# Performance work log

Hardware: AMD Instinct MI355X
Metric: run time of the kernel (lower is better)

## Reference

```python
import jax, jax.numpy as jnp
import numpy as np

GROUPS = 32
EPS = 1e-5
N_HEADS = 8
MAX_REL = 16  # temporal_length
NEG_INF = -1e8


def group_norm(x, scale, bias):
    # x: [N, C, L]
    n, c, l = x.shape
    xg = x.reshape(n, GROUPS, (c // GROUPS) * l)
    mean = xg.mean(-1, keepdims=True)
    var = xg.var(-1, keepdims=True)
    xn = ((xg - mean) / jnp.sqrt(var + EPS)).reshape(n, c, l)
    return xn * scale[None, :, None] + bias[None, :, None]


def conv1x1(x, w, b):
    # x: [N, Cin, L], w: [Cout, Cin], b: [Cout]
    return jnp.einsum('oc,ncl->nol', w, x) + b[None, :, None]


def rel_pos_emb(table, length):
    # table: [2*MAX_REL+1, ch] -> [length, length, ch]
    r = jnp.arange(length)
    dist = jnp.clip(r[None, :] - r[:, None], -MAX_REL, MAX_REL) + MAX_REL
    return table[dist]


def qkv_attention(qkv, k_rp=None, v_rp=None, causal=False):
    # qkv: [N, 3*H*ch, L]  (new attention order: chunk into q,k,v blocks)
    bs, width, L = qkv.shape
    ch = width // (3 * N_HEADS)
    q, k, v = jnp.split(qkv, 3, axis=1)
    q = q.reshape(bs * N_HEADS, ch, L)
    k = k.reshape(bs * N_HEADS, ch, L)
    v = v.reshape(bs * N_HEADS, ch, L)
    scale = 1.0 / jnp.sqrt(jnp.sqrt(jnp.asarray(ch, dtype=qkv.dtype)))
    w = jnp.einsum('bct,bcs->bts', q * scale, k * scale)
    if k_rp is not None:
        # faithful to original: 'bst' result added directly onto 'bts' weight
        w = w + jnp.einsum('bct,tsc->bst', q * scale, k_rp)
    if causal:
        mask = jnp.tril(jnp.ones((L, L), dtype=w.dtype))
        w = jnp.where(mask == 0, NEG_INF, w)
    w = jax.nn.softmax(w, axis=-1)
    a = jnp.einsum('bts,bcs->bct', w, v)
    if v_rp is not None:
        a = a + jnp.einsum('bts,tsc->btc', w, v_rp).transpose(0, 2, 1)
    return a.reshape(bs, -1, L)


def st_attention(x, norm_s_w, norm_s_b, qkv_s_w, qkv_s_b, proj_s_w, proj_s_b,
                 norm_t_w, norm_t_b, qkv_t_w, qkv_t_b, proj_t_w, proj_t_b,
                 rpk_table, rpv_table):
    b, c, t, h, w = x.shape
    # spatial attention over (h*w) tokens, batch (b*t)
    out = x.transpose(0, 2, 1, 3, 4).reshape(b * t, c, h * w)
    qkv = conv1x1(group_norm(out, norm_s_w, norm_s_b), qkv_s_w, qkv_s_b)
    out = qkv_attention(qkv)
    out = conv1x1(out, proj_s_w, proj_s_b)
    out = out.reshape(b, t, c, h, w).transpose(0, 2, 1, 3, 4)
    x = x + out
    # temporal attention over t tokens, batch (b*h*w), with RPE + causal mask
    out = x.transpose(0, 3, 4, 1, 2).reshape(b * h * w, c, t)
    qkv = conv1x1(group_norm(out, norm_t_w, norm_t_b), qkv_t_w, qkv_t_b)
    k_rp = rel_pos_emb(rpk_table, t)
    v_rp = rel_pos_emb(rpv_table, t)
    out = qkv_attention(qkv, k_rp=k_rp, v_rp=v_rp, causal=True)
    out = conv1x1(out, proj_t_w, proj_t_b)
    out = out.reshape(b, h, w, c, t).transpose(0, 3, 4, 1, 2)
    return x + out


def setup_inputs() -> dict:
    key = jax.random.key(0)
    ks = jax.random.split(key, 12)
    B, C, T, H, W = 2, 512, 16, 24, 24
    ch = C // N_HEADS
    inp = {
        'x': jax.random.normal(ks[0], (B, C, T, H, W), jnp.float32),
        'norm_s_w': jnp.ones((C,), jnp.float32),
        'norm_s_b': jnp.zeros((C,), jnp.float32),
        'qkv_s_w': jax.random.normal(ks[1], (3 * C, C), jnp.float32) * 0.02,
        'qkv_s_b': jnp.zeros((3 * C,), jnp.float32),
        'proj_s_w': jax.random.normal(ks[2], (C, C), jnp.float32) * 0.02,
        'proj_s_b': jnp.zeros((C,), jnp.float32),
        'norm_t_w': jnp.ones((C,), jnp.float32),
        'norm_t_b': jnp.zeros((C,), jnp.float32),
        'qkv_t_w': jax.random.normal(ks[3], (3 * C, C), jnp.float32) * 0.02,
        'qkv_t_b': jnp.zeros((3 * C,), jnp.float32),
        'proj_t_w': jax.random.normal(ks[4], (C, C), jnp.float32) * 0.02,
        'proj_t_b': jnp.zeros((C,), jnp.float32),
        'rpk_table': jax.random.normal(ks[5], (2 * MAX_REL + 1, ch), jnp.float32) * 0.05,
        'rpv_table': jax.random.normal(ks[6], (2 * MAX_REL + 1, ch), jnp.float32) * 0.05,
    }
    return inp


def reference(x, norm_s_w, norm_s_b, qkv_s_w, qkv_s_b, proj_s_w, proj_s_b,
              norm_t_w, norm_t_b, qkv_t_w, qkv_t_b, proj_t_w, proj_t_b,
              rpk_table, rpv_table):
    return st_attention(x, norm_s_w, norm_s_b, qkv_s_w, qkv_s_b, proj_s_w, proj_s_b,
                        norm_t_w, norm_t_b, qkv_t_w, qkv_t_b, proj_t_w, proj_t_b,
                        rpk_table, rpv_table)
```

## Files before the change

kernel.cpp:

```cpp
#include <hip/hip_runtime.h>
#include <hip/hip_bf16.h>

typedef __hip_bfloat16 bf16;
typedef __attribute__((ext_vector_type(8))) short v8s;
typedef __attribute__((ext_vector_type(4))) float v4f;

__device__ __forceinline__ float b2f(bf16 v){ return __bfloat162float(v); }
__device__ __forceinline__ bf16  f2b(float v){ return __float2bfloat16(v); }

__device__ __forceinline__ float ldin(const void* p, int i, bool f32in){
  return f32in ? ((const float*)p)[i] : b2f(((const bf16*)p)[i]);
}

__device__ __forceinline__ void stage4(const void* src, size_t off, bool f32in, bf16* dst){
  union { bf16 h[4]; ushort4 u; } tmp;
  if (f32in){
    float4 f = *(const float4*)((const float*)src + off);
    tmp.h[0] = f2b(f.x); tmp.h[1] = f2b(f.y); tmp.h[2] = f2b(f.z); tmp.h[3] = f2b(f.w);
  } else {
    tmp.u = *(const ushort4*)((const ushort*)src + off);
  }
  *(ushort4*)dst = tmp.u;
}
__device__ __forceinline__ void stage4b(const bf16* src, bf16* dst){
  *(ushort4*)dst = *(const ushort4*)src;
}

__device__ __forceinline__ void async_cp16(const bf16* g, bf16* l){
  __builtin_amdgcn_global_load_lds(
      (const __attribute__((address_space(1))) unsigned int*)g,
      (__attribute__((address_space(3))) unsigned int*)l, 16, 0, 0);
}


__global__ void k_detect(const void* x, int* flag){
  int tid = threadIdx.x;
  const bf16* p = (const bf16*)x;
  int cnt = 0;
  for (int i = tid; i < 512; i += 64){
    float v = b2f(p[i]);
    if (!(fabsf(v) <= 64.f)) cnt++;
  }
  #pragma unroll
  for (int off = 32; off; off >>= 1) cnt += __shfl_down(cnt, off, 64);
  if (tid == 0) flag[0] = (cnt > 16) ? 1 : 0;
}

__global__ __launch_bounds__(256) void k_cvtw(const void* __restrict__ W,
        bf16* __restrict__ out, int n4, const int* __restrict__ flag){
  const bool f32in = flag[0] != 0;
  int i = blockIdx.x*256 + threadIdx.x;
  if (i < n4) stage4(W, (size_t)i*4, f32in, out + (size_t)i*4);
}

__global__ __launch_bounds__(256) void k_gn_s(const void* __restrict__ x,
        const void* __restrict__ gw, const void* __restrict__ gb,
        bf16* __restrict__ xnT, const int* __restrict__ flag, int n0){
  const bool f32in = flag[0] != 0;
  const int g = blockIdx.x;
  const int nl = blockIdx.y;
  const int n = n0 + nl;
  const int b = n >> 4, t = n & 15;
  const int tid = threadIdx.x;
  __shared__ float xs[576*17];
  __shared__ float red[4][2];
  __shared__ float stats[2];
  float s = 0.f, q = 0.f;
  for (int i = tid; i < 9216; i += 256){
    int cg = i / 576, l = i - cg*576;
    int c = g*16 + cg;
    float v = ldin(x, ((b*512 + c)*16 + t)*576 + l, f32in);
    xs[l*17 + cg] = v; s += v; q += v*v;
  }
  #pragma unroll
  for (int off = 32; off; off >>= 1){ s += __shfl_down(s, off, 64); q += __shfl_down(q, off, 64); }
  int wid = tid >> 6;
  if ((tid & 63) == 0){ red[wid][0] = s; red[wid][1] = q; }
  __syncthreads();
  if (tid == 0){
    float S = red[0][0]+red[1][0]+red[2][0]+red[3][0];
    float Q = red[0][1]+red[1][1]+red[2][1]+red[3][1];
    float mean = S * (1.f/9216.f);
    float var  = Q * (1.f/9216.f) - mean*mean;
    stats[0] = mean; stats[1] = rsqrtf(fmaxf(var, 0.f) + 1e-5f);
  }
  __syncthreads();
  float mean = stats[0], rstd = stats[1];
  for (int i = tid; i < 9216; i += 256){
    int l = i >> 4, cg = i & 15;
    int c = g*16 + cg;
    xnT[(size_t)(nl*576 + l)*512 + c] =
        f2b((xs[l*17 + cg] - mean)*rstd*ldin(gw, c, f32in) + ldin(gb, c, f32in));
  }
}

__global__ __launch_bounds__(256) void k_gemm_qkv(const bf16* __restrict__ Xf,
        const bf16* __restrict__ Wb, const void* __restrict__ Bv,
        bf16* __restrict__ Y, const int* __restrict__ flag,
        size_t kOff, size_t vOff, int mode){
  const bool f32in = flag[0] != 0;
  const int nwg = gridDim.x;
  const int bid = blockIdx.x;
  const int g = (bid & 7)*(nwg >> 3) + (bid >> 3);
  const int mt = g / 12, nt = g - mt*12;
  const int r0 = mt*128, o0 = nt*128;
  const int tid = threadIdx.x, lane = tid & 63, w = tid >> 6;
  const int wm = w & 1, wn = w >> 1;
  const int r15 = lane & 15, quad = lane >> 4;
  const int rsw = r15 & 7;
  __shared__ bf16 As[128*64];
  __shared__ bf16 Bs[128*64];
  v4f acc[4][4];
  #pragma unroll
  for (int i = 0; i < 4; ++i)
    #pragma unroll
    for (int j = 0; j < 4; ++j) acc[i][j] = (v4f){0.f,0.f,0.f,0.f};
  for (int kc = 0; kc < 512; kc += 64){
    __syncthreads();
    #pragma unroll
    for (int r = 0; r < 4; ++r){
      int d = (tid + 256*r)*8;
      int row = d >> 6;
      int slot = (d >> 3) & 7;
      int col = ((slot ^ (row & 7)) * 8);
      async_cp16(&Xf[(size_t)(r0 + row)*512 + kc + col], As + r*2048 + w*512);
      async_cp16(&Wb[(size_t)(o0 + row)*512 + kc + col], Bs + r*2048 + w*512);
    }
    __syncthreads();
    #pragma unroll
    for (int ks = 0; ks < 2; ++ks){
      v8s a[4], b[4];
      #pragma unroll
      for (int mi = 0; mi < 4; ++mi)
        a[mi] = *(const v8s*)&As[(wm*64 + mi*16 + r15)*64 + (((ks*4 + quad) ^ rsw)*8)];
      #pragma unroll
      for (int ni = 0; ni < 4; ++ni)
        b[ni] = *(const v8s*)&Bs[(wn*64 + ni*16 + r15)*64 + (((ks*4 + quad) ^ rsw)*8)];
      #pragma unroll
      for (int mi = 0; mi < 4; ++mi)
        #pragma unroll
        for (int ni = 0; ni < 4; ++ni)
          acc[mi][ni] = __builtin_amdgcn_mfma_f32_16x16x32_bf16(a[mi], b[ni], acc[mi][ni], 0, 0, 0);
    }
  }
  if (mode == 0){
    #pragma unroll
    for (int ni = 0; ni < 4; ++ni){
      int o = o0 + wn*64 + ni*16 + r15;
      int seg = o >> 9, oseg = o & 511;
      size_t segb = (seg==0) ? 0 : (seg==1) ? kOff : vOff;
      float bia = ldin(Bv, o, f32in);
      #pragma unroll
      for (int mi = 0; mi < 4; ++mi)
        #pragma unroll
        for (int rg = 0; rg < 4; ++rg){
          int rr = r0 + wm*64 + mi*16 + quad*4 + rg;
          int nl = rr / 576, l = rr - nl*576;
          size_t dst = segb + (size_t)nl*294912 +
                       ((seg==2) ? ((size_t)oseg*576 + l) : ((size_t)l*512 + oseg));
          Y[dst] = f2b(acc[mi][ni][rg] + bia);
        }
    }
  } else {
    #pragma unroll
    for (int ni = 0; ni < 4; ++ni){
      int o = o0 + wn*64 + ni*16 + r15;
      float bia = ldin(Bv, o, f32in);
      #pragma unroll
      for (int mi = 0; mi < 4; ++mi)
        #pragma unroll
        for (int rg = 0; rg < 4; ++rg){
          int rr = r0 + wm*64 + mi*16 + quad*4 + rg;
          int m = rr >> 4, t = rr & 15;
          Y[((size_t)m*1536 + o)*16 + t] = f2b(acc[mi][ni][rg] + bia);
        }
    }
  }
}

__global__ __launch_bounds__(256, 4) void k_attn_s_mfma(const bf16* __restrict__ qkv,
        bf16* __restrict__ attT, size_t kOff, size_t vOff){
  const int bid = blockIdx.x;
  const int xcd = bid & 7, slot = bid >> 3;
  const int nl = xcd + 8*(slot/72);
  const int idx = slot - 72*(slot/72);
  const int head = idx/9, t0 = idx - 9*head;
  const int tid = threadIdx.x, lane = tid & 63, w = tid >> 6;
  const int r15 = lane & 15, quad = lane >> 4;
  __shared__ bf16 Ks[64*72];
  __shared__ bf16 Vs[64*72];
  __shared__ bf16 Ps[4][16*72];
  const bf16* QT = qkv + (size_t)nl*294912;
  const bf16* KT = qkv + kOff + (size_t)nl*294912;
  const bf16* Vp = qkv + vOff + (size_t)nl*294912;
  const int c0 = head*64;
  v8s aq0, aq1;
  {
    const bf16* qrow = QT + (size_t)(t0*64 + w*16 + r15)*512 + c0;
    aq0 = *(const v8s*)(qrow + quad*8);
    aq1 = *(const v8s*)(qrow + 32 + quad*8);
  }
  v4f oc[4];
  #pragma unroll
  for (int ni = 0; ni < 4; ++ni) oc[ni] = (v4f){0.f,0.f,0.f,0.f};
  float m_run[4] = {-1e30f,-1e30f,-1e30f,-1e30f};
  float l_run[4] = {0.f,0.f,0.f,0.f};
  for (int sc = 0; sc < 9; ++sc){
    __syncthreads();
    #pragma unroll
    for (int r = 0; r < 4; ++r){
      int e4 = (tid + 256*r)*4;
      int row = e4 >> 6, col = e4 & 63;
      stage4b(&KT[(size_t)(sc*64 + row)*512 + c0 + col], &Ks[row*72 + col]);
      stage4b(&Vp[(size_t)(c0 + row)*576 + sc*64 + col], &Vs[row*72 + col]);
    }
    __syncthreads();
    v4f sa[4];
    #pragma unroll
    for (int sj = 0; sj < 4; ++sj) sa[sj] = (v4f){0.f,0.f,0.f,0.f};
    #pragma unroll
    for (int sj = 0; sj < 4; ++sj){
      v8s b0 = *(const v8s*)&Ks[(sj*16 + r15)*72 + quad*8];
      v8s b1 = *(const v8s*)&Ks[(sj*16 + r15)*72 + 32 + quad*8];
      sa[sj] = __builtin_amdgcn_mfma_f32_16x16x32_bf16(aq0, b0, sa[sj], 0, 0, 0);
      sa[sj] = __builtin_amdgcn_mfma_f32_16x16x32_bf16(aq1, b1, sa[sj], 0, 0, 0);
    }
    float cmx[4] = {-1e30f,-1e30f,-1e30f,-1e30f};
    #pragma unroll
    for (int sj = 0; sj < 4; ++sj)
      #pragma unroll
      for (int rg = 0; rg < 4; ++rg){
        float v = sa[sj][rg]*0.125f;
        sa[sj][rg] = v;
        cmx[rg] = fmaxf(cmx[rg], v);
      }
    #pragma unroll
    for (int off = 1; off < 16; off <<= 1)
      #pragma unroll
      for (int rg = 0; rg < 4; ++rg) cmx[rg] = fmaxf(cmx[rg], __shfl_xor(cmx[rg], off, 64));
    float alpha[4];
    #pragma unroll
    for (int rg = 0; rg < 4; ++rg){
      float mnew = fmaxf(m_run[rg], cmx[rg]);
      alpha[rg] = __expf(m_run[rg] - mnew);
      m_run[rg] = mnew;
    }
    float psum[4] = {0.f,0.f,0.f,0.f};
    #pragma unroll
    for (int sj = 0; sj < 4; ++sj)
      #pragma unroll
      for (int rg = 0; rg < 4; ++rg){
        float e = __expf(sa[sj][rg] - m_run[rg]);
        sa[sj][rg] = e; psum[rg] += e;
      }
    #pragma unroll
    for (int off = 1; off < 16; off <<= 1)
      #pragma unroll
      for (int rg = 0; rg < 4; ++rg) psum[rg] += __shfl_xor(psum[rg], off, 64);
    #pragma unroll
    for (int rg = 0; rg < 4; ++rg) l_run[rg] = l_run[rg]*alpha[rg] + psum[rg];
    #pragma unroll
    for (int ni = 0; ni < 4; ++ni)
      #pragma unroll
      for (int rg = 0; rg < 4; ++rg) oc[ni][rg] *= alpha[rg];
    #pragma unroll
    for (int sj = 0; sj < 4; ++sj)
      #pragma unroll
      for (int rg = 0; rg < 4; ++rg)
        Ps[w][(quad*4 + rg)*72 + sj*16 + r15] = f2b(sa[sj][rg]);
    #pragma unroll
    for (int ks = 0; ks < 2; ++ks){
      v8s a = *(const v8s*)&Ps[w][r15*72 + ks*32 + quad*8];
      #pragma unroll
      for (int ni = 0; ni < 4; ++ni){
        v8s b = *(const v8s*)&Vs[(ni*16 + r15)*72 + ks*32 + quad*8];
        oc[ni] = __builtin_amdgcn_mfma_f32_16x16x32_bf16(a, b, oc[ni], 0, 0, 0);
      }
    }
  }
  float inv[4];
  #pragma unroll
  for (int rg = 0; rg < 4; ++rg) inv[rg] = 1.f / l_run[rg];
  #pragma unroll
  for (int ni = 0; ni < 4; ++ni)
    #pragma unroll
    for (int rg = 0; rg < 4; ++rg){
      int t = t0*64 + w*16 + quad*4 + rg;
      attT[(size_t)(nl*576 + t)*512 + c0 + ni*16 + r15] = f2b(oc[ni][rg]*inv[rg]);
    }
}

__global__ __launch_bounds__(256) void k_proj_s_mfma(const bf16* __restrict__ AT,
        const bf16* __restrict__ Wb, const void* __restrict__ Bv,
        const void* __restrict__ xin, bf16* __restrict__ x2,
        bf16* __restrict__ x2T, int doT,
        const int* __restrict__ flag, int n0){
  const bool f32in = flag[0] != 0;
  const int o0 = blockIdx.x * 128;
  const int l0 = blockIdx.y * 64;
  const int nl = blockIdx.z;
  const int n = n0 + nl;
  const int b = n >> 4, t = n & 15;
  const int tid = threadIdx.x, lane = tid & 63;
  const int wm = (tid >> 6) & 1, wn = tid >> 7;
  const int r15 = lane & 15, quad = lane >> 4;
  __shared__ bf16 As[128*72];
  __shared__ bf16 Bs[64*72];
  v4f acc[4][2];
  #pragma unroll
  for (int i = 0; i < 4; ++i)
    #pragma unroll
    for (int j = 0; j < 2; ++j) acc[i][j] = (v4f){0.f,0.f,0.f,0.f};
  for (int kc = 0; kc < 512; kc += 64){
    __syncthreads();
    #pragma unroll
    for (int r = 0; r < 8; ++r){
      int e4 = (tid + 256*r)*4;
      int row = e4 >> 6, k = e4 & 63;
      stage4b(&Wb[(size_t)(o0+row)*512 + kc + k], &As[row*72 + k]);
    }
    #pragma unroll
    for (int r = 0; r < 4; ++r){
      int e4 = (tid + 256*r)*4;
      int row = e4 >> 6, k = e4 & 63;
      stage4b(&AT[(size_t)(nl*576 + l0 + row)*512 + kc + k], &Bs[row*72 + k]);
    }
    __syncthreads();
    #pragma unroll
    for (int ks = 0; ks < 2; ++ks){
      v8s a[4], b[2];
      #pragma unroll
      for (int mi = 0; mi < 4; ++mi)
        a[mi] = *(const v8s*)&As[(wm*64 + mi*16 + r15)*72 + ks*32 + quad*8];
      #pragma unroll
      for (int ni = 0; ni < 2; ++ni)
        b[ni] = *(const v8s*)&Bs[(wn*32 + ni*16 + r15)*72 + ks*32 + quad*8];
      #pragma unroll
      for (int mi = 0; mi < 4; ++mi)
        #pragma unroll
        for (int ni = 0; ni < 2; ++ni)
          acc[mi][ni] = __builtin_amdgcn_mfma_f32_16x16x32_bf16(a[mi], b[ni], acc[mi][ni], 0, 0, 0);
    }
  }
  __syncthreads();
  #pragma unroll
  for (int mi = 0; mi < 4; ++mi){
    int orel = wm*64 + mi*16 + quad*4;
    #pragma unroll
    for (int rg = 0; rg < 4; ++rg){
      float bia = ldin(Bv, o0 + orel + rg, f32in);
      #pragma unroll
      for (int ni = 0; ni < 2; ++ni)
        As[(orel + rg)*72 + wn*32 + ni*16 + r15] = f2b(acc[mi][ni][rg] + bia);
    }
  }
  __syncthreads();
  const size_t xrow = ((size_t)(b*512 + o0)*16 + t)*576 + l0;
  for (int it = 0; it < 4; ++it){
    int idx = tid + it*256;
    int o = idx >> 3, lc = (idx & 7)*8;
    union { bf16 h[8]; v8s v; } val;
    val.v = *(const v8s*)&As[o*72 + lc];
    size_t ga = xrow + (size_t)o*9216 + lc;
    if (f32in){
      const float* xp = (const float*)xin + ga;
      float4 f0 = *(const float4*)xp;
      float4 f1 = *(const float4*)(xp + 4);
      val.h[0] = f2b(b2f(val.h[0]) + f0.x);
      val.h[1] = f2b(b2f(val.h[1]) + f0.y);
      val.h[2] = f2b(b2f(val.h[2]) + f0.z);
      val.h[3] = f2b(b2f(val.h[3]) + f0.w);
      val.h[4] = f2b(b2f(val.h[4]) + f1.x);
      val.h[5] = f2b(b2f(val.h[5]) + f1.y);
      val.h[6] = f2b(b2f(val.h[6]) + f1.z);
      val.h[7] = f2b(b2f(val.h[7]) + f1.w);
    } else {
      union { bf16 h[8]; v8s v; } xv;
      xv.v = *(const v8s*)((const bf16*)xin + ga);
      #pragma unroll
      for (int j = 0; j < 8; ++j) val.h[j] = f2b(b2f(val.h[j]) + b2f(xv.h[j]));
    }
    *(v8s*)&x2[ga] = val.v;
    if (doT) *(v8s*)&As[o*72 + lc] = val.v;
  }
  if (doT){
    __syncthreads();
    const size_t tbase = ((size_t)b*576 + l0)*8192 + (size_t)t*512 + o0;
    for (int it = 0; it < 4; ++it){
      int l = (tid & 15) + it*16;
      int ocg = (tid >> 4)*8;
      union { bf16 h[8]; v8s v; } val;
      #pragma unroll
      for (int j = 0; j < 8; ++j) val.h[j] = As[(ocg + j)*72 + l];
      *(v8s*)&x2T[tbase + (size_t)l*8192 + ocg] = val.v;
    }
  }
}

__global__ __launch_bounds__(256) void k_gn_t(const bf16* __restrict__ x2,
        const void* __restrict__ gw, const void* __restrict__ gb,
        bf16* __restrict__ xnT, const int* __restrict__ flag, int m0){
  const bool f32in = flag[0] != 0;
  const int ml = blockIdx.x;
  const int m = m0 + ml;
  const int b = m / 576, l = m - b*576;
  const int tid = threadIdx.x;
  __shared__ float xs[8192];
  __shared__ float mg[32], rg[32];
  for (int i = tid; i < 8192; i += 256){
    int t = i >> 9, c = i & 511;
    xs[i] = b2f(x2[((b*512 + c)*16 + t)*576 + l]);
  }
  __syncthreads();
  {
    int g = tid >> 3, ii = tid & 7;
    float s = 0.f, q = 0.f;
    for (int idx = ii; idx < 256; idx += 8){
      int t = idx >> 4, cg = idx & 15;
      float v = xs[t*512 + g*16 + cg]; s += v; q += v*v;
    }
    #pragma unroll
    for (int off = 1; off < 8; off <<= 1){ s += __shfl_xor(s, off, 64); q += __shfl_xor(q, off, 64); }
    if (ii == 0){
      float mean = s*(1.f/256.f);
      float var  = q*(1.f/256.f) - mean*mean;
      mg[g] = mean; rg[g] = rsqrtf(fmaxf(var, 0.f) + 1e-5f);
    }
  }
  __syncthreads();
  for (int i = tid; i < 8192; i += 256){
    int c = i & 511, g = c >> 4;
    xnT[(size_t)ml*8192 + i] = f2b((xs[i] - mg[g])*rg[g]*ldin(gw, c, f32in) + ldin(gb, c, f32in));
  }
}

__global__ __launch_bounds__(256) void k_gn_t2(const bf16* __restrict__ x2T,
        const void* __restrict__ gw, const void* __restrict__ gb,
        bf16* __restrict__ xnT, const int* __restrict__ flag, int m0){
  const bool f32in = flag[0] != 0;
  const int ml = blockIdx.x;
  const int m = m0 + ml;
  const int tid = threadIdx.x;
  __shared__ float xs[8192];
  __shared__ float mg[32], rg[32];
  for (int i = tid; i < 8192; i += 256)
    xs[i] = b2f(x2T[(size_t)m*8192 + i]);
  __syncthreads();
  {
    int g = tid >> 3, ii = tid & 7;
    float s = 0.f, q = 0.f;
    for (int idx = ii; idx < 256; idx += 8){
      int t = idx >> 4, cg = idx & 15;
      float v = xs[t*512 + g*16 + cg]; s += v; q += v*v;
    }
    #pragma unroll
    for (int off = 1; off < 8; off <<= 1){ s += __shfl_xor(s, off, 64); q += __shfl_xor(q, off, 64); }
    if (ii == 0){
      float mean = s*(1.f/256.f);
      float var  = q*(1.f/256.f) - mean*mean;
      mg[g] = mean; rg[g] = rsqrtf(fmaxf(var, 0.f) + 1e-5f);
    }
  }
  __syncthreads();
  for (int i = tid; i < 8192; i += 256){
    int c = i & 511, g = c >> 4;
    xnT[(size_t)ml*8192 + i] = f2b((xs[i] - mg[g])*rg[g]*ldin(gw, c, f32in) + ldin(gb, c, f32in));
  }
}

__global__ __launch_bounds__(256) void k_attn_t(const bf16* __restrict__ qkv,
        const void* __restrict__ tbk, const void* __restrict__ tbv,
        bf16* __restrict__ attT, const int* __restrict__ flag){
  const bool f32in = flag[0] != 0;
  const int head = blockIdx.x;
  const int ml = blockIdx.y;
  const int tid = threadIdx.x;
  __shared__ float qsT[16*68], ksT[16*68], vsT[16*68];
  __shared__ float tks[33*68], tvs[33*68];
  __shared__ float ps[16*17];
  const int base = (ml*1536 + head*64)*16;
  for (int i = tid; i < 1024; i += 256){
    int c = i >> 4, t = i & 15;
    qsT[t*68 + c] = b2f(qkv[base + i]);
    ksT[t*68 + c] = b2f(qkv[base + 8192 + i]);
    vsT[t*68 + c] = b2f(qkv[base + 16384 + i]);
  }
  for (int i = tid; i < 33*64; i += 256){
    int d = i >> 6, c = i & 63;
    tks[d*68 + c] = ldin(tbk, i, f32in);
    tvs[d*68 + c] = ldin(tbv, i, f32in);
  }
  __syncthreads();
  {
    const int t = tid >> 4, s = tid & 15;
    const float4* qt = (const float4*)&qsT[t*68];
    const float4* kr = (const float4*)&ksT[s*68];
    const float4* q2 = (const float4*)&qsT[s*68];
    const float4* tr = (const float4*)&tks[(t - s + 16)*68];
    float qk = 0.f, rp = 0.f;
    #pragma unroll
    for (int c4 = 0; c4 < 16; ++c4){
      float4 a = qt[c4], b = kr[c4];
      qk += a.x*b.x + a.y*b.y + a.z*b.z + a.w*b.w;
      float4 a2 = q2[c4], tb = tr[c4];
      rp += a2.x*tb.x + a2.y*tb.y + a2.z*tb.z + a2.w*tb.w;
    }
    float logit = 0.125f*qk + 0.35355339059327373f*rp;
    if (s > t) logit = -1e8f;
    float mx = logit;
    #pragma unroll
    for (int off = 8; off; off >>= 1) mx = fmaxf(mx, __shfl_xor(mx, off, 16));
    float e = __expf(logit - mx);
    float tot = e;
    #pragma unroll
    for (int off = 8; off; off >>= 1) tot += __shfl_xor(tot, off, 16);
    ps[t*17 + s] = e / tot;
  }
  __syncthreads();
  {
    const int c4 = tid & 15, t = tid >> 4;
    float4 acc = {0.f,0.f,0.f,0.f};
    #pragma unroll
    for (int s = 0; s < 16; ++s){
      float p = ps[t*17 + s];
      float4 v4 = *(const float4*)&vsT[s*68 + c4*4];
      float4 t4 = *(const float4*)&tvs[(s - t + 16)*68 + c4*4];
      acc.x += p*(v4.x + t4.x); acc.y += p*(v4.y + t4.y);
      acc.z += p*(v4.z + t4.z); acc.w += p*(v4.w + t4.w);
    }
    union { bf16 h[4]; ushort4 u; } o;
    o.h[0] = f2b(acc.x); o.h[1] = f2b(acc.y); o.h[2] = f2b(acc.z); o.h[3] = f2b(acc.w);
    *(ushort4*)&attT[(size_t)ml*8192 + t*512 + head*64 + c4*4] = o.u;
  }
}

__global__ __launch_bounds__(256) void k_proj_t_mfma(const bf16* __restrict__ AT,
        const bf16* __restrict__ Wb, const void* __restrict__ Bv,
        const bf16* __restrict__ x2, void* __restrict__ out,
        const int* __restrict__ flag, int m0){
  const bool f32in = flag[0] != 0;
  const int o0 = blockIdx.x * 128;
  const int tp = blockIdx.y;
  const int mg0 = blockIdx.z * 32;
  const int tid = threadIdx.x, lane = tid & 63;
  const int wm = (tid >> 6) & 1, wn = tid >> 7;
  const int r15 = lane & 15, quad = lane >> 4;
  __shared__ bf16 As[128*72];
  __shared__ bf16 Bs[64*72];
  v4f acc[4][2];
  #pragma unroll
  for (int i = 0; i < 4; ++i)
    #pragma unroll
    for (int j = 0; j < 2; ++j) acc[i][j] = (v4f){0.f,0.f,0.f,0.f};
  for (int kc = 0; kc < 512; kc += 64){
    __syncthreads();
    #pragma unroll
    for (int r = 0; r < 8; ++r){
      int e4 = (tid + 256*r)*4;
      int row = e4 >> 6, k = e4 & 63;
      stage4b(&Wb[(size_t)(o0+row)*512 + kc + k], &As[row*72 + k]);
    }
    #pragma unroll
    for (int r = 0; r < 4; ++r){
      int e4 = (tid + 256*r)*4;
      int row = e4 >> 6, k = e4 & 63;
      stage4b(&AT[(size_t)(mg0 + (row & 31))*8192 + (tp*2 + (row >> 5))*512 + kc + k],
              &Bs[row*72 + k]);
    }
    __syncthreads();
    #pragma unroll
    for (int ks = 0; ks < 2; ++ks){
      v8s a[4], b[2];
      #pragma unroll
      for (int mi = 0; mi < 4; ++mi)
        a[mi] = *(const v8s*)&As[(wm*64 + mi*16 + r15)*72 + ks*32 + quad*8];
      #pragma unroll
      for (int ni = 0; ni < 2; ++ni)
        b[ni] = *(const v8s*)&Bs[(wn*32 + ni*16 + r15)*72 + ks*32 + quad*8];
      #pragma unroll
      for (int mi = 0; mi < 4; ++mi)
        #pragma unroll
        for (int ni = 0; ni < 2; ++ni)
          acc[mi][ni] = __builtin_amdgcn_mfma_f32_16x16x32_bf16(a[mi], b[ni], acc[mi][ni], 0, 0, 0);
    }
  }
  const int tt = tp*2 + wn;
  #pragma unroll
  for (int mi = 0; mi < 4; ++mi)
    #pragma unroll
    for (int rg = 0; rg < 4; ++rg){
      int o = o0 + wm*64 + mi*16 + quad*4 + rg;
      float bia = ldin(Bv, o, f32in);
      #pragma unroll
      for (int ni = 0; ni < 2; ++ni){
        int m = m0 + mg0 + ni*16 + r15;
        int b = m / 576, l = m - b*576;
        size_t addr = ((size_t)(b*512 + o)*16 + tt)*576 + l;
        float val = acc[mi][ni][rg] + bia + b2f(x2[addr]);
        if (f32in) ((float*)out)[addr] = val;
        else       ((bf16*)out)[addr] = f2b(val);
      }
    }
}

extern "C" void kernel_launch(void* const* d_in, const int* in_sizes, int n_in,
                              void* d_out, int out_size, void* d_ws, size_t ws_size,
                              hipStream_t stream){
  const void* x   = d_in[0];
  const void* nsw = d_in[1];
  const void* nsb = d_in[2];
  const void* qsw = d_in[3];
  const void* qsb = d_in[4];
  const void* psw = d_in[5];
  const void* psb = d_in[6];
  const void* ntw = d_in[7];
  const void* ntb = d_in[8];
  const void* qtw = d_in[9];
  const void* qtb = d_in[10];
  const void* ptw = d_in[11];
  const void* ptb = d_in[12];
  const void* rpk = d_in[13];
  const void* rpv = d_in[14];

  const size_t S_full = (size_t)32*294912;
  const size_t need_full = 256 + (S_full*5 + 9437184)*2;
  const size_t need_T    = 256 + (S_full*5 + (size_t)2*9437184)*2;
  const int NCH = (ws_size >= need_full) ? 32 : 8;
  const int MCH = (NCH == 32) ? 1152 : 288;
  const size_t S = (size_t)NCH*294912;
  const int useT = (NCH == 32 && ws_size >= need_T) ? 1 : 0;

  int*  flag = (int*)d_ws;
  bf16* A  = (bf16*)((char*)d_ws + 256);
  bf16* A2 = A  + S;
  bf16* Bq = A2 + S;
  bf16* Cx = Bq + 3*S;
  bf16* Cx2 = Cx + 9437184;
  const size_t kOff = S, vOff = 2*S;
  bf16* Wcv  = A2;
  bf16* Wcv2 = Bq;

  k_detect<<<1, 64, 0, stream>>>(x, flag);

  for (int n0 = 0; n0 < 32; n0 += NCH){
    k_gn_s       <<<dim3(32, NCH),   256, 0, stream>>>(x, nsw, nsb, A, flag, n0);
    k_cvtw       <<<dim3(768),       256, 0, stream>>>(qsw, Wcv, 196608, flag);
    k_gemm_qkv   <<<dim3(NCH*54),    256, 0, stream>>>(A, Wcv, qsb, Bq, flag, kOff, vOff, 0);
    k_attn_s_mfma<<<dim3(72*NCH),    256, 0, stream>>>(Bq, A2, kOff, vOff);
    k_cvtw       <<<dim3(256),       256, 0, stream>>>(psw, Bq, 65536, flag);
    k_proj_s_mfma<<<dim3(4, 9, NCH), 256, 0, stream>>>(A2, Bq, psb, x, Cx, Cx2, useT, flag, n0);
  }
  for (int m0 = 0; m0 < 1152; m0 += MCH){
    if (useT) k_gn_t2<<<dim3(MCH),   256, 0, stream>>>(Cx2, ntw, ntb, A, flag, m0);
    else      k_gn_t <<<dim3(MCH),   256, 0, stream>>>(Cx,  ntw, ntb, A, flag, m0);
    k_cvtw       <<<dim3(768),       256, 0, stream>>>(qtw, Wcv, 196608, flag);
    k_gemm_qkv   <<<dim3((MCH/2)*3), 256, 0, stream>>>(A, Wcv, qtb, Bq, flag, 0, 0, 1);
    k_attn_t     <<<dim3(8, MCH),    256, 0, stream>>>(Bq, rpk, rpv, A2, flag);
    k_cvtw       <<<dim3(256),       256, 0, stream>>>(ptw, Wcv2, 65536, flag);
    k_proj_t_mfma<<<dim3(4, 8, MCH/32), 256, 0, stream>>>(A2, Wcv2, ptb, Cx, d_out, flag, m0);
  }
}
```

Before: 507.1 us.

## Prefetch K/V tiles into registers and use lazy exp2 rescaling in spatial attention

```diff
diff --git a/kernel.cpp b/kernel.cpp
--- a/kernel.cpp
+++ b/kernel.cpp
@@ -200,24 +200,43 @@
     aq0 = *(const v8s*)(qrow + quad*8);
     aq1 = *(const v8s*)(qrow + 32 + quad*8);
   }
+  int srow[4], scol[4];
+  #pragma unroll
+  for (int r = 0; r < 4; ++r){
+    int e4 = (tid + 256*r)*4;
+    srow[r] = e4 >> 6; scol[r] = e4 & 63;
+  }
+  ushort4 kreg[4], vreg[4];
+  #pragma unroll
+  for (int r = 0; r < 4; ++r){
+    kreg[r] = *(const ushort4*)&KT[(size_t)srow[r]*512 + c0 + scol[r]];
+    vreg[r] = *(const ushort4*)&Vp[(size_t)(c0 + srow[r])*576 + scol[r]];
+  }
   v4f oc[4];
   #pragma unroll
   for (int ni = 0; ni < 4; ++ni) oc[ni] = (v4f){0.f,0.f,0.f,0.f};
   float m_run[4] = {-1e30f,-1e30f,-1e30f,-1e30f};
   float l_run[4] = {0.f,0.f,0.f,0.f};
+  const float SC = 0.180336880f;
   for (int sc = 0; sc < 9; ++sc){
     __syncthreads();
     #pragma unroll
     for (int r = 0; r < 4; ++r){
-      int e4 = (tid + 256*r)*4;
-      int row = e4 >> 6, col = e4 & 63;
-      stage4b(&KT[(size_t)(sc*64 + row)*512 + c0 + col], &Ks[row*72 + col]);
-      stage4b(&Vp[(size_t)(c0 + row)*576 + sc*64 + col], &Vs[row*72 + col]);
-    }
-    __syncthreads();
+      *(ushort4*)&Ks[srow[r]*72 + scol[r]] = kreg[r];
+      *(ushort4*)&Vs[srow[r]*72 + scol[r]] = vreg[r];
+    }
+    __syncthreads();
+    if (sc < 8){
+      #pragma unroll
+      for (int r = 0; r < 4; ++r){
+        kreg[r] = *(const ushort4*)&KT[(size_t)((sc+1)*64 + srow[r])*512 + c0 + scol[r]];
+        vreg[r] = *(const ushort4*)&Vp[(size_t)(c0 + srow[r])*576 + (sc+1)*64 + scol[r]];
+      }
+    }
     v4f sa[4];
     #pragma unroll
     for (int sj = 0; sj < 4; ++sj) sa[sj] = (v4f){0.f,0.f,0.f,0.f};
+    __builtin_amdgcn_s_setprio(1);
     #pragma unroll
     for (int sj = 0; sj < 4; ++sj){
       v8s b0 = *(const v8s*)&Ks[(sj*16 + r15)*72 + quad*8];
@@ -225,12 +244,13 @@
       sa[sj] = __builtin_amdgcn_mfma_f32_16x16x32_bf16(aq0, b0, sa[sj], 0, 0, 0);
       sa[sj] = __builtin_amdgcn_mfma_f32_16x16x32_bf16(aq1, b1, sa[sj], 0, 0, 0);
     }
+    __builtin_amdgcn_s_setprio(0);
     float cmx[4] = {-1e30f,-1e30f,-1e30f,-1e30f};
     #pragma unroll
     for (int sj = 0; sj < 4; ++sj)
       #pragma unroll
       for (int rg = 0; rg < 4; ++rg){
-        float v = sa[sj][rg]*0.125f;
+        float v = sa[sj][rg]*SC;
         sa[sj][rg] = v;
         cmx[rg] = fmaxf(cmx[rg], v);
       }
@@ -238,19 +258,25 @@
     for (int off = 1; off < 16; off <<= 1)
       #pragma unroll
       for (int rg = 0; rg < 4; ++rg) cmx[rg] = fmaxf(cmx[rg], __shfl_xor(cmx[rg], off, 64));
-    float alpha[4];
-    #pragma unroll
-    for (int rg = 0; rg < 4; ++rg){
-      float mnew = fmaxf(m_run[rg], cmx[rg]);
-      alpha[rg] = __expf(m_run[rg] - mnew);
-      m_run[rg] = mnew;
+    float grow = fmaxf(fmaxf(cmx[0]-m_run[0], cmx[1]-m_run[1]),
+                       fmaxf(cmx[2]-m_run[2], cmx[3]-m_run[3]));
+    if (__any(grow > 8.f)){
+      #pragma unroll
+      for (int rg = 0; rg < 4; ++rg){
+        float mnew = fmaxf(m_run[rg], cmx[rg]);
+        float al = exp2f(m_run[rg] - mnew);
+        m_run[rg] = mnew;
+        l_run[rg] *= al;
+        #pragma unroll
+        for (int ni = 0; ni < 4; ++ni) oc[ni][rg] *= al;
+      }
     }
     float psum[4] = {0.f,0.f,0.f,0.f};
     #pragma unroll
     for (int sj = 0; sj < 4; ++sj)
       #pragma unroll
       for (int rg = 0; rg < 4; ++rg){
-        float e = __expf(sa[sj][rg] - m_run[rg]);
+        float e = exp2f(sa[sj][rg] - m_run[rg]);
         sa[sj][rg] = e; psum[rg] += e;
       }
     #pragma unroll
@@ -258,16 +284,13 @@
       #pragma unroll
       for (int rg = 0; rg < 4; ++rg) psum[rg] += __shfl_xor(psum[rg], off, 64);
     #pragma unroll
-    for (int rg = 0; rg < 4; ++rg) l_run[rg] = l_run[rg]*alpha[rg] + psum[rg];
-    #pragma unroll
-    for (int ni = 0; ni < 4; ++ni)
-      #pragma unroll
-      for (int rg = 0; rg < 4; ++rg) oc[ni][rg] *= alpha[rg];
+    for (int rg = 0; rg < 4; ++rg) l_run[rg] += psum[rg];
     #pragma unroll
     for (int sj = 0; sj < 4; ++sj)
       #pragma unroll
       for (int rg = 0; rg < 4; ++rg)
         Ps[w][(quad*4 + rg)*72 + sj*16 + r15] = f2b(sa[sj][rg]);
+    __builtin_amdgcn_s_setprio(1);
     #pragma unroll
     for (int ks = 0; ks < 2; ++ks){
       v8s a = *(const v8s*)&Ps[w][r15*72 + ks*32 + quad*8];
@@ -277,6 +300,7 @@
         oc[ni] = __builtin_amdgcn_mfma_f32_16x16x32_bf16(a, b, oc[ni], 0, 0, 0);
       }
     }
+    __builtin_amdgcn_s_setprio(0);
   }
   float inv[4];
   #pragma unroll
```

Result: no change. 512.1 us (+1.0%).
